# Kernel tuning notes

Hardware: AMD Instinct MI355X
Metric: run time of the kernel (lower is better)

## Reference

```python
import jax, jax.numpy as jnp
import numpy as np

B, N, M_PARAM, F_IN, HEADS, HID, OUT, MLP_H, N_ACT = 64, 512, 50, 3, 2, 3, 3, 128, 512
NEG_SLOPE = 0.2


def setup_inputs() -> dict:
    key = jax.random.key(0)
    ks = jax.random.split(key, 20)
    s = 0.1
    idx = jax.random.uniform(ks[0], (B, N), dtype=jnp.float32)
    x = jax.random.normal(ks[1], (B, N, F_IN), dtype=jnp.float32)
    y = jax.random.normal(ks[2], (B, M_PARAM + 2, F_IN), dtype=jnp.float32)
    adj = (jax.random.uniform(ks[3], (B, N, N)) < 0.02).astype(jnp.float32)
    # GATConv 1: in=3 -> heads=2, out=3 (concat)
    W1 = jax.random.normal(ks[4], (F_IN, HEADS * HID), dtype=jnp.float32) * s
    a_src1 = jax.random.normal(ks[5], (HEADS, HID), dtype=jnp.float32) * s
    a_dst1 = jax.random.normal(ks[6], (HEADS, HID), dtype=jnp.float32) * s
    b1 = jnp.zeros((HEADS * HID,), dtype=jnp.float32)
    # GATConv 2: in=6 -> heads=1, out=3
    W2 = jax.random.normal(ks[7], (HEADS * HID, OUT), dtype=jnp.float32) * s
    a_src2 = jax.random.normal(ks[8], (1, OUT), dtype=jnp.float32) * s
    a_dst2 = jax.random.normal(ks[9], (1, OUT), dtype=jnp.float32) * s
    b2 = jnp.zeros((OUT,), dtype=jnp.float32)
    fc_in = N + N * OUT + (M_PARAM + 2) * 3  # 2204
    Wf1 = jax.random.normal(ks[10], (fc_in, MLP_H), dtype=jnp.float32) * (1.0 / np.sqrt(fc_in))
    bf1 = jnp.zeros((MLP_H,), dtype=jnp.float32)
    Wf2 = jax.random.normal(ks[11], (MLP_H, N_ACT), dtype=jnp.float32) * (1.0 / np.sqrt(MLP_H))
    bf2 = jnp.zeros((N_ACT,), dtype=jnp.float32)
    return {"idx": idx, "x": x, "y": y, "adj": adj,
            "W1": W1, "a_src1": a_src1, "a_dst1": a_dst1, "b1": b1,
            "W2": W2, "a_src2": a_src2, "a_dst2": a_dst2, "b2": b2,
            "Wf1": Wf1, "bf1": bf1, "Wf2": Wf2, "bf2": bf2}


def gat_layer(x, adj, W, a_src, a_dst, bias):
    # PyG GATConv (concat=True): h = x W; alpha_ij = softmax_i(leaky_relu(a_src.h_i + a_dst.h_j))
    # edge (i -> j) exists iff adj[i, j] != 0; self-loops added per PyG default.
    Bb, Nn = x.shape[0], x.shape[1]
    Hh, D = a_src.shape
    h = (x @ W).reshape(Bb, Nn, Hh, D)                     # [B,N,H,D]
    es = jnp.einsum('bnhd,hd->bnh', h, a_src)              # source term
    ed = jnp.einsum('bnhd,hd->bnh', h, a_dst)              # target term
    logits = es[:, :, None, :] + ed[:, None, :, :]         # [B, i(src), j(dst), H]
    logits = jax.nn.leaky_relu(logits, NEG_SLOPE)
    mask = (adj > 0) | jnp.eye(Nn, dtype=bool)[None]       # self-loops
    logits = jnp.where(mask[..., None], logits, jnp.float32(-1e9))
    alpha = jax.nn.softmax(logits, axis=1)                 # softmax over sources per target
    out = jnp.einsum('bijh,bihd->bjhd', alpha, h)          # aggregate at targets
    return out.reshape(Bb, Nn, Hh * D) + bias


def reference(idx, x, y, adj, W1, a_src1, a_dst1, b1, W2, a_src2, a_dst2, b2, Wf1, bf1, Wf2, bf2):
    g = jax.nn.relu(gat_layer(x, adj, W1, a_src1, a_dst1, b1))
    g = gat_layer(g, adj, W2, a_src2, a_dst2, b2)          # heads=1
    feat = jnp.concatenate([idx.reshape(B, -1), g.reshape(B, -1), y.reshape(B, -1)], axis=-1)
    h = jax.nn.relu(feat @ Wf1 + bf1)
    return h @ Wf2 + bf2
```

## Files before the change

kernel.cpp:

```cpp
#include <hip/hip_runtime.h>
#include <hip/hip_bf16.h>
#include <stdint.h>

#define B_    64
#define N_    512
#define M2    52
#define MLPH  128
#define NACT  512
#define FC_IN 2204
#define NCH   18
#define NEG   0.2f
#define NW    16

__device__ __forceinline__ float lrelu(float v){ return v > 0.f ? v : NEG * v; }

__global__ __launch_bounds__(512) void kfuse1(const float* __restrict__ adj,
                                              const float* __restrict__ x,
                                              const float* __restrict__ W1,
                                              const float* __restrict__ as1,
                                              const float* __restrict__ ad1,
                                              const float* __restrict__ b1,
                                              const float* __restrict__ W2,
                                              const float* __restrict__ as2,
                                              uint32_t* __restrict__ maskT,
                                              float* __restrict__ node2){
  __shared__ uint32_t lm[2][64][16];
  __shared__ float node[N_][8];
  int b  = blockIdx.y;
  int j0 = blockIdx.x * 64;
  int t  = threadIdx.x;

  {
    int j4 = t & 15;
    int w  = (t >> 4) & 15;
    int kh = t >> 8;
    const float* basef = adj + ((size_t)(b * N_ + (w << 5) + (kh << 4))) * N_ + (j0 + (j4 << 2));
    uint32_t m0 = 0, m1 = 0, m2 = 0, m3 = 0;
#pragma unroll
    for (int k = 0; k < 16; ++k) {
      float4 v = *(const float4*)(basef + (size_t)k * N_);
      m0 |= (v.x > 0.f ? 1u : 0u) << k;
      m1 |= (v.y > 0.f ? 1u : 0u) << k;
      m2 |= (v.z > 0.f ? 1u : 0u) << k;
      m3 |= (v.w > 0.f ? 1u : 0u) << k;
    }
    int sh = kh << 4;
    lm[kh][(j4 << 2) + 0][w] = m0 << sh;
    lm[kh][(j4 << 2) + 1][w] = m1 << sh;
    lm[kh][(j4 << 2) + 2][w] = m2 << sh;
    lm[kh][(j4 << 2) + 3][w] = m3 << sh;
  }

  {
    float xv0 = x[((size_t)(b * N_ + t)) * 3 + 0];
    float xv1 = x[((size_t)(b * N_ + t)) * 3 + 1];
    float xv2 = x[((size_t)(b * N_ + t)) * 3 + 2];
    float h[6];
#pragma unroll
    for (int c = 0; c < 6; ++c) h[c] = xv0 * W1[c] + xv1 * W1[6 + c] + xv2 * W1[12 + c];
#pragma unroll
    for (int c = 0; c < 6; ++c) node[t][c] = h[c];
    node[t][6] = h[0] * as1[0] + h[1] * as1[1] + h[2] * as1[2];
    node[t][7] = h[3] * as1[3] + h[4] * as1[4] + h[5] * as1[5];
  }
  __syncthreads();

  int w  = t & 15;
  int tg = t >> 4;
  float ad10 = ad1[0], ad11 = ad1[1], ad12 = ad1[2];
  float ad13 = ad1[3], ad14 = ad1[4], ad15 = ad1[5];
  float b10 = b1[0], b11 = b1[1], b12 = b1[2], b13 = b1[3], b14 = b1[4], b15 = b1[5];
  float as20 = as2[0], as21 = as2[1], as22 = as2[2];

#pragma unroll
  for (int p = 0; p < 2; ++p) {
    int jj = tg + p * 32;
    int j  = j0 + jj;
    uint32_t bits = lm[0][jj][w] | lm[1][jj][w];
    maskT[((size_t)(b * N_ + j)) * NW + w] = bits;
    if ((j >> 5) == w) bits |= 1u << (j & 31);

    float ed0 = node[j][0] * ad10 + node[j][1] * ad11 + node[j][2] * ad12;
    float ed1 = node[j][3] * ad13 + node[j][4] * ad14 + node[j][5] * ad15;

    float den0 = 0.f, den1 = 0.f;
    float a0 = 0.f, a1 = 0.f, a2 = 0.f, a3 = 0.f, a4 = 0.f, a5 = 0.f;
    while (bits) {
      int k = __ffs(bits) - 1;
      bits &= bits - 1;
      int i = (w << 5) + k;
      float e0 = __expf(lrelu(node[i][6] + ed0));
      float e1 = __expf(lrelu(node[i][7] + ed1));
      den0 += e0; den1 += e1;
      a0 += e0 * node[i][0]; a1 += e0 * node[i][1]; a2 += e0 * node[i][2];
      a3 += e1 * node[i][3]; a4 += e1 * node[i][4]; a5 += e1 * node[i][5];
    }
#pragma unroll
    for (int m = 1; m < 16; m <<= 1) {
      den0 += __shfl_xor(den0, m); den1 += __shfl_xor(den1, m);
      a0 += __shfl_xor(a0, m); a1 += __shfl_xor(a1, m); a2 += __shfl_xor(a2, m);
      a3 += __shfl_xor(a3, m); a4 += __shfl_xor(a4, m); a5 += __shfl_xor(a5, m);
    }
    float r0 = 1.f / den0, r1 = 1.f / den1;
    float g0 = fmaxf(a0 * r0 + b10, 0.f);
    float g1v = fmaxf(a1 * r0 + b11, 0.f);
    float g2v = fmaxf(a2 * r0 + b12, 0.f);
    float g3 = fmaxf(a3 * r1 + b13, 0.f);
    float g4 = fmaxf(a4 * r1 + b14, 0.f);
    float g5 = fmaxf(a5 * r1 + b15, 0.f);
    float h20 = g0*W2[0] + g1v*W2[3] + g2v*W2[6] + g3*W2[9]  + g4*W2[12] + g5*W2[15];
    float h21 = g0*W2[1] + g1v*W2[4] + g2v*W2[7] + g3*W2[10] + g4*W2[13] + g5*W2[16];
    float h22 = g0*W2[2] + g1v*W2[5] + g2v*W2[8] + g3*W2[11] + g4*W2[14] + g5*W2[17];
    float es2 = h20 * as20 + h21 * as21 + h22 * as22;
    if (w < 4) {
      float outv = (w == 0) ? h20 : (w == 1) ? h21 : (w == 2) ? h22 : es2;
      node2[((size_t)(b * N_ + j)) * 4 + w] = outv;
    }
  }
}

__global__ __launch_bounds__(256) void kagg2(const float* __restrict__ node2,
                                             const float* __restrict__ ad2,
                                             const float* __restrict__ b2,
                                             const uint32_t* __restrict__ maskT,
                                             float* __restrict__ g2){
  __shared__ float sn[N_][4];
  int b = blockIdx.y, tile = blockIdx.x, t = threadIdx.x;

  const float4* src = (const float4*)(node2 + (size_t)b * N_ * 4);
  for (int e = t; e < N_; e += 256) {
    float4 v = src[e];
    sn[e][0] = v.x; sn[e][1] = v.y; sn[e][2] = v.z; sn[e][3] = v.w;
  }
  __syncthreads();

  int w = t & 15, tg = t >> 4;
  int j = tile * 16 + tg;
  float ad20 = ad2[0], ad21 = ad2[1], ad22 = ad2[2];

  uint32_t bits = maskT[((size_t)(b * N_ + j)) * NW + w];
  if ((j >> 5) == w) bits |= 1u << (j & 31);

  float ed = sn[j][0] * ad20 + sn[j][1] * ad21 + sn[j][2] * ad22;
  float den = 0.f, a0 = 0.f, a1 = 0.f, a2 = 0.f;
  while (bits) {
    int k = __ffs(bits) - 1;
    bits &= bits - 1;
    int i = (w << 5) + k;
    float e = __expf(lrelu(sn[i][3] + ed));
    den += e;
    a0 += e * sn[i][0]; a1 += e * sn[i][1]; a2 += e * sn[i][2];
  }
#pragma unroll
  for (int m = 1; m < 16; m <<= 1) {
    den += __shfl_xor(den, m);
    a0 += __shfl_xor(a0, m); a1 += __shfl_xor(a1, m); a2 += __shfl_xor(a2, m);
  }
  if (w < 3) {
    float r = 1.f / den;
    float v = (w == 0 ? a0 : w == 1 ? a1 : a2) * r + b2[w];
    g2[((size_t)(b * N_ + j)) * 3 + w] = v;
  }
}

__global__ __launch_bounds__(128) void kmlp1(const float* __restrict__ idx,
                                             const float* __restrict__ y,
                                             const float* __restrict__ g2,
                                             const float* __restrict__ Wf1,
                                             float* __restrict__ partial){
  __shared__ float fs[128];
  int c = blockIdx.x, b = blockIdx.y, t = threadIdx.x;
  int k = c * 128 + t;
  float v = 0.f;
  if (k < FC_IN) {
    if (k < N_)            v = idx[(size_t)b * N_ + k];
    else if (k < N_ * 4)   v = g2[(size_t)b * (N_ * 3) + (k - N_)];
    else                   v = y[(size_t)b * (M2 * 3) + (k - N_ * 4)];
  }
  fs[t] = v;
  __syncthreads();
  int klen = min(128, FC_IN - c * 128);
  const float* wp = Wf1 + (size_t)(c * 128) * MLPH + t;
  float p = 0.f;
#pragma unroll 8
  for (int kk = 0; kk < klen; ++kk) p += fs[kk] * wp[(size_t)kk * MLPH];
  partial[((size_t)b * NCH + c) * MLPH + t] = p;
}

__global__ __launch_bounds__(128) void kmlp2(const float* __restrict__ partial,
                                             const float* __restrict__ bf1,
                                             const float* __restrict__ Wf2,
                                             const float* __restrict__ bf2,
                                             float* __restrict__ out){
  __shared__ float hid[MLPH];
  int q = blockIdx.x, b = blockIdx.y, t = threadIdx.x;
  float s = bf1[t];
  const float* pp = partial + (size_t)b * NCH * MLPH + t;
#pragma unroll
  for (int c = 0; c < NCH; ++c) s += pp[c * MLPH];
  hid[t] = fmaxf(s, 0.f);
  __syncthreads();
  int o = q * 128 + t;
  float acc = bf2[o];
  const float* wp = Wf2 + o;
#pragma unroll 8
  for (int k = 0; k < MLPH; ++k) acc += hid[k] * wp[(size_t)k * NACT];
  out[(size_t)b * NACT + o] = acc;
}

extern "C" void kernel_launch(void* const* d_in, const int* in_sizes, int n_in,
                              void* d_out, int out_size, void* d_ws, size_t ws_size,
                              hipStream_t stream) {
  const float* idx = (const float*)d_in[0];
  const float* x   = (const float*)d_in[1];
  const float* y   = (const float*)d_in[2];
  const float* adj = (const float*)d_in[3];
  const float* W1  = (const float*)d_in[4];
  const float* as1 = (const float*)d_in[5];
  const float* ad1 = (const float*)d_in[6];
  const float* b1  = (const float*)d_in[7];
  const float* W2  = (const float*)d_in[8];
  const float* as2 = (const float*)d_in[9];
  const float* ad2 = (const float*)d_in[10];
  const float* b2  = (const float*)d_in[11];
  const float* Wf1 = (const float*)d_in[12];
  const float* bf1 = (const float*)d_in[13];
  const float* Wf2 = (const float*)d_in[14];
  const float* bf2 = (const float*)d_in[15];
  float* out = (float*)d_out;

  uint8_t* ws = (uint8_t*)d_ws;
  uint32_t* maskT = (uint32_t*)ws;
  float* node2    = (float*)(ws + 2097152);
  float* g2       = (float*)(ws + 2097152 + 524288);
  float* partial  = (float*)(ws + 2097152 + 524288 + 393216);

  hipLaunchKernelGGL(kfuse1, dim3(8, B_),   dim3(512), 0, stream,
                     adj, x, W1, as1, ad1, b1, W2, as2, maskT, node2);
  hipLaunchKernelGGL(kagg2,  dim3(32, B_),  dim3(256), 0, stream,
                     node2, ad2, b2, maskT, g2);
  hipLaunchKernelGGL(kmlp1,  dim3(NCH, B_), dim3(128), 0, stream, idx, y, g2, Wf1, partial);
  hipLaunchKernelGGL(kmlp2,  dim3(4, B_),   dim3(128), 0, stream, partial, bf1, Wf2, bf2, out);
}
```

Baseline: 38.44 us.

## Fuse second GAT aggregation into first MLP layer kernel

```diff
diff --git a/kernel.cpp b/kernel.cpp
--- a/kernel.cpp
+++ b/kernel.cpp
@@ -119,66 +119,71 @@
   }
 }
 
-__global__ __launch_bounds__(256) void kagg2(const float* __restrict__ node2,
-                                             const float* __restrict__ ad2,
-                                             const float* __restrict__ b2,
-                                             const uint32_t* __restrict__ maskT,
-                                             float* __restrict__ g2){
+__global__ __launch_bounds__(128) void kmlp1f(const float* __restrict__ idx,
+                                              const float* __restrict__ y,
+                                              const float* __restrict__ node2,
+                                              const float* __restrict__ ad2,
+                                              const float* __restrict__ b2,
+                                              const uint32_t* __restrict__ maskT,
+                                              const float* __restrict__ Wf1,
+                                              float* __restrict__ partial){
   __shared__ float sn[N_][4];
-  int b = blockIdx.y, tile = blockIdx.x, t = threadIdx.x;
-
-  const float4* src = (const float4*)(node2 + (size_t)b * N_ * 4);
-  for (int e = t; e < N_; e += 256) {
-    float4 v = src[e];
-    sn[e][0] = v.x; sn[e][1] = v.y; sn[e][2] = v.z; sn[e][3] = v.w;
-  }
-  __syncthreads();
-
-  int w = t & 15, tg = t >> 4;
-  int j = tile * 16 + tg;
-  float ad20 = ad2[0], ad21 = ad2[1], ad22 = ad2[2];
-
-  uint32_t bits = maskT[((size_t)(b * N_ + j)) * NW + w];
-  if ((j >> 5) == w) bits |= 1u << (j & 31);
-
-  float ed = sn[j][0] * ad20 + sn[j][1] * ad21 + sn[j][2] * ad22;
-  float den = 0.f, a0 = 0.f, a1 = 0.f, a2 = 0.f;
-  while (bits) {
-    int k = __ffs(bits) - 1;
-    bits &= bits - 1;
-    int i = (w << 5) + k;
-    float e = __expf(lrelu(sn[i][3] + ed));
-    den += e;
-    a0 += e * sn[i][0]; a1 += e * sn[i][1]; a2 += e * sn[i][2];
-  }
-#pragma unroll
-  for (int m = 1; m < 16; m <<= 1) {
-    den += __shfl_xor(den, m);
-    a0 += __shfl_xor(a0, m); a1 += __shfl_xor(a1, m); a2 += __shfl_xor(a2, m);
-  }
-  if (w < 3) {
-    float r = 1.f / den;
-    float v = (w == 0 ? a0 : w == 1 ? a1 : a2) * r + b2[w];
-    g2[((size_t)(b * N_ + j)) * 3 + w] = v;
-  }
-}
-
-__global__ __launch_bounds__(128) void kmlp1(const float* __restrict__ idx,
-                                             const float* __restrict__ y,
-                                             const float* __restrict__ g2,
-                                             const float* __restrict__ Wf1,
-                                             float* __restrict__ partial){
+  __shared__ float gloc[44][3];
   __shared__ float fs[128];
   int c = blockIdx.x, b = blockIdx.y, t = threadIdx.x;
-  int k = c * 128 + t;
-  float v = 0.f;
-  if (k < FC_IN) {
+
+  if (c >= 4 && c < 16) {
+    const float4* src = (const float4*)(node2 + (size_t)b * N_ * 4);
+    for (int e = t; e < N_; e += 128) {
+      float4 v = src[e];
+      sn[e][0] = v.x; sn[e][1] = v.y; sn[e][2] = v.z; sn[e][3] = v.w;
+    }
+    __syncthreads();
+
+    int kg0 = c * 128 - 512;
+    int j0n = kg0 / 3;
+    int j1n = (kg0 + 127) / 3;
+    int w = t & 15, grp = t >> 4;
+    float ad20 = ad2[0], ad21 = ad2[1], ad22 = ad2[2];
+    float b20 = b2[0], b21 = b2[1], b22 = b2[2];
+
+    for (int jj = j0n + grp; jj <= j1n; jj += 8) {
+      uint32_t bits = maskT[((size_t)(b * N_ + jj)) * NW + w];
+      if ((jj >> 5) == w) bits |= 1u << (jj & 31);
+      float ed = sn[jj][0] * ad20 + sn[jj][1] * ad21 + sn[jj][2] * ad22;
+      float den = 0.f, a0 = 0.f, a1 = 0.f, a2 = 0.f;
+      while (bits) {
+        int k = __ffs(bits) - 1;
+        bits &= bits - 1;
+        int i = (w << 5) + k;
+        float e = __expf(lrelu(sn[i][3] + ed));
+        den += e;
+        a0 += e * sn[i][0]; a1 += e * sn[i][1]; a2 += e * sn[i][2];
+      }
+#pragma unroll
+      for (int m = 1; m < 16; m <<= 1) {
+        den += __shfl_xor(den, m);
+        a0 += __shfl_xor(a0, m); a1 += __shfl_xor(a1, m); a2 += __shfl_xor(a2, m);
+      }
+      if (w < 3) {
+        float r = 1.f / den;
+        float v = (w == 0 ? a0 : w == 1 ? a1 : a2) * r + (w == 0 ? b20 : w == 1 ? b21 : b22);
+        gloc[jj - j0n][w] = v;
+      }
+    }
+    __syncthreads();
+    int kg = kg0 + t;
+    int j = kg / 3, comp = kg - 3 * j;
+    fs[t] = gloc[j - j0n][comp];
+  } else {
+    int k = c * 128 + t;
+    float v = 0.f;
     if (k < N_)            v = idx[(size_t)b * N_ + k];
-    else if (k < N_ * 4)   v = g2[(size_t)b * (N_ * 3) + (k - N_)];
-    else                   v = y[(size_t)b * (M2 * 3) + (k - N_ * 4)];
-  }
-  fs[t] = v;
+    else if (k >= 2048 && k < FC_IN) v = y[(size_t)b * (M2 * 3) + (k - 2048)];
+    fs[t] = v;
+  }
   __syncthreads();
+
   int klen = min(128, FC_IN - c * 128);
   const float* wp = Wf1 + (size_t)(c * 128) * MLPH + t;
   float p = 0.f;
@@ -232,13 +237,12 @@
   uint8_t* ws = (uint8_t*)d_ws;
   uint32_t* maskT = (uint32_t*)ws;
   float* node2    = (float*)(ws + 2097152);
-  float* g2       = (float*)(ws + 2097152 + 524288);
-  float* partial  = (float*)(ws + 2097152 + 524288 + 393216);
+  float* partial  = (float*)(ws + 2097152 + 524288);
 
   hipLaunchKernelGGL(kfuse1, dim3(8, B_),   dim3(512), 0, stream,
                      adj, x, W1, as1, ad1, b1, W2, as2, maskT, node2);
-  hipLaunchKernelGGL(kagg2,  dim3(32, B_),  dim3(256), 0, stream,
-                     node2, ad2, b2, maskT, g2);
-  hipLaunchKernelGGL(kmlp1,  dim3(NCH, B_), dim3(128), 0, stream, idx, y, g2, Wf1, partial);
-  hipLaunchKernelGGL(kmlp2,  dim3(4, B_),   dim3(128), 0, stream, partial, bf1, Wf2, bf2, out);
-}
+  hipLaunchKernelGGL(kmlp1f, dim3(NCH, B_), dim3(128), 0, stream,
+                     idx, y, node2, ad2, b2, maskT, Wf1, partial);
+  hipLaunchKernelGGL(kmlp2,  dim3(4, B_),   dim3(128), 0, stream,
+                     partial, bf1, Wf2, bf2, out);
+}
```

Result: slower. 39.84 us (+3.6%).

## Fuse layer-2 aggregation and both MLP layers into one per-batch kernel

Applied to the files above, without the earlier changes.

```diff
diff --git a/kernel.cpp b/kernel.cpp
--- a/kernel.cpp
+++ b/kernel.cpp
@@ -8,7 +8,6 @@
 #define MLPH  128
 #define NACT  512
 #define FC_IN 2204
-#define NCH   18
 #define NEG   0.2f
 #define NW    16
 
@@ -119,93 +118,116 @@
   }
 }
 
-__global__ __launch_bounds__(256) void kagg2(const float* __restrict__ node2,
-                                             const float* __restrict__ ad2,
-                                             const float* __restrict__ b2,
-                                             const uint32_t* __restrict__ maskT,
-                                             float* __restrict__ g2){
+__global__ __launch_bounds__(1024) void kback(const float* __restrict__ idx,
+                                              const float* __restrict__ y,
+                                              const float* __restrict__ node2,
+                                              const float* __restrict__ ad2,
+                                              const float* __restrict__ b2,
+                                              const uint32_t* __restrict__ maskT,
+                                              const float* __restrict__ Wf1,
+                                              const float* __restrict__ bf1,
+                                              const float* __restrict__ Wf2,
+                                              const float* __restrict__ bf2,
+                                              float* __restrict__ out){
+  __shared__ uint32_t smask[N_][NW];
   __shared__ float sn[N_][4];
-  int b = blockIdx.y, tile = blockIdx.x, t = threadIdx.x;
-
-  const float4* src = (const float4*)(node2 + (size_t)b * N_ * 4);
-  for (int e = t; e < N_; e += 256) {
-    float4 v = src[e];
-    sn[e][0] = v.x; sn[e][1] = v.y; sn[e][2] = v.z; sn[e][3] = v.w;
-  }
-  __syncthreads();
-
-  int w = t & 15, tg = t >> 4;
-  int j = tile * 16 + tg;
-  float ad20 = ad2[0], ad21 = ad2[1], ad22 = ad2[2];
-
-  uint32_t bits = maskT[((size_t)(b * N_ + j)) * NW + w];
-  if ((j >> 5) == w) bits |= 1u << (j & 31);
-
-  float ed = sn[j][0] * ad20 + sn[j][1] * ad21 + sn[j][2] * ad22;
-  float den = 0.f, a0 = 0.f, a1 = 0.f, a2 = 0.f;
-  while (bits) {
-    int k = __ffs(bits) - 1;
-    bits &= bits - 1;
-    int i = (w << 5) + k;
-    float e = __expf(lrelu(sn[i][3] + ed));
-    den += e;
-    a0 += e * sn[i][0]; a1 += e * sn[i][1]; a2 += e * sn[i][2];
-  }
-#pragma unroll
-  for (int m = 1; m < 16; m <<= 1) {
-    den += __shfl_xor(den, m);
-    a0 += __shfl_xor(a0, m); a1 += __shfl_xor(a1, m); a2 += __shfl_xor(a2, m);
-  }
-  if (w < 3) {
-    float r = 1.f / den;
-    float v = (w == 0 ? a0 : w == 1 ? a1 : a2) * r + b2[w];
-    g2[((size_t)(b * N_ + j)) * 3 + w] = v;
-  }
-}
-
-__global__ __launch_bounds__(128) void kmlp1(const float* __restrict__ idx,
-                                             const float* __restrict__ y,
-                                             const float* __restrict__ g2,
-                                             const float* __restrict__ Wf1,
-                                             float* __restrict__ partial){
-  __shared__ float fs[128];
-  int c = blockIdx.x, b = blockIdx.y, t = threadIdx.x;
-  int k = c * 128 + t;
-  float v = 0.f;
-  if (k < FC_IN) {
-    if (k < N_)            v = idx[(size_t)b * N_ + k];
-    else if (k < N_ * 4)   v = g2[(size_t)b * (N_ * 3) + (k - N_)];
-    else                   v = y[(size_t)b * (M2 * 3) + (k - N_ * 4)];
-  }
-  fs[t] = v;
-  __syncthreads();
-  int klen = min(128, FC_IN - c * 128);
-  const float* wp = Wf1 + (size_t)(c * 128) * MLPH + t;
-  float p = 0.f;
+  __shared__ float feat[2208];
+  __shared__ float red[4096];
+  __shared__ float hid[MLPH];
+  int b = blockIdx.x, t = threadIdx.x;
+
+  {
+    const uint4* src = (const uint4*)(maskT + (size_t)b * N_ * NW);
+    uint4* dst = (uint4*)smask;
+    dst[t] = src[t];
+    dst[t + 1024] = src[t + 1024];
+  }
+  if (t < 512) {
+    float4 v = ((const float4*)(node2 + (size_t)b * N_ * 4))[t];
+    sn[t][0] = v.x; sn[t][1] = v.y; sn[t][2] = v.z; sn[t][3] = v.w;
+    feat[t] = idx[(size_t)b * N_ + t];
+  } else if (t < 512 + M2 * 3) {
+    feat[2048 + (t - 512)] = y[(size_t)b * (M2 * 3) + (t - 512)];
+  }
+  __syncthreads();
+
+  {
+    int w = t & 15, jt = t >> 4;
+    float ad20 = ad2[0], ad21 = ad2[1], ad22 = ad2[2];
+    float b20 = b2[0], b21 = b2[1], b22 = b2[2];
+#pragma unroll
+    for (int r = 0; r < 8; ++r) {
+      int j = r * 64 + jt;
+      uint32_t bits = smask[j][w];
+      if ((j >> 5) == w) bits |= 1u << (j & 31);
+      float ed = sn[j][0] * ad20 + sn[j][1] * ad21 + sn[j][2] * ad22;
+      float den = 0.f, a0 = 0.f, a1 = 0.f, a2 = 0.f;
+      while (bits) {
+        int k = __ffs(bits) - 1;
+        bits &= bits - 1;
+        int i = (w << 5) + k;
+        float e = __expf(lrelu(sn[i][3] + ed));
+        den += e;
+        a0 += e * sn[i][0]; a1 += e * sn[i][1]; a2 += e * sn[i][2];
+      }
+#pragma unroll
+      for (int m = 1; m < 16; m <<= 1) {
+        den += __shfl_xor(den, m);
+        a0 += __shfl_xor(a0, m); a1 += __shfl_xor(a1, m); a2 += __shfl_xor(a2, m);
+      }
+      if (w < 3) {
+        float r_ = 1.f / den;
+        float v = (w == 0 ? a0 : w == 1 ? a1 : a2) * r_ + (w == 0 ? b20 : w == 1 ? b21 : b22);
+        feat[N_ + 3 * j + w] = v;
+      }
+    }
+  }
+  __syncthreads();
+
+  {
+    int kq = t >> 5, ug = t & 31;
+    int kstart = kq * 69;
+    int klen = min(69, FC_IN - kstart);
+    const float4* wrow = (const float4*)(Wf1 + (size_t)kstart * MLPH) + ug;
+    float a0 = 0.f, a1 = 0.f, a2 = 0.f, a3 = 0.f;
 #pragma unroll 8
-  for (int kk = 0; kk < klen; ++kk) p += fs[kk] * wp[(size_t)kk * MLPH];
-  partial[((size_t)b * NCH + c) * MLPH + t] = p;
-}
-
-__global__ __launch_bounds__(128) void kmlp2(const float* __restrict__ partial,
-                                             const float* __restrict__ bf1,
-                                             const float* __restrict__ Wf2,
-                                             const float* __restrict__ bf2,
-                                             float* __restrict__ out){
-  __shared__ float hid[MLPH];
-  int q = blockIdx.x, b = blockIdx.y, t = threadIdx.x;
-  float s = bf1[t];
-  const float* pp = partial + (size_t)b * NCH * MLPH + t;
-#pragma unroll
-  for (int c = 0; c < NCH; ++c) s += pp[c * MLPH];
-  hid[t] = fmaxf(s, 0.f);
-  __syncthreads();
-  int o = q * 128 + t;
-  float acc = bf2[o];
-  const float* wp = Wf2 + o;
-#pragma unroll 8
-  for (int k = 0; k < MLPH; ++k) acc += hid[k] * wp[(size_t)k * NACT];
-  out[(size_t)b * NACT + o] = acc;
+    for (int k2 = 0; k2 < 69; ++k2) {
+      if (k2 < klen) {
+        float fv = feat[kstart + k2];
+        float4 w = wrow[(size_t)k2 * 32];
+        a0 += fv * w.x; a1 += fv * w.y; a2 += fv * w.z; a3 += fv * w.w;
+      }
+    }
+    ((float4*)red)[kq * 32 + ug] = make_float4(a0, a1, a2, a3);
+  }
+  __syncthreads();
+  if (t < MLPH) {
+    float s = bf1[t];
+#pragma unroll
+    for (int q = 0; q < 32; ++q) s += red[q * MLPH + t];
+    hid[t] = fmaxf(s, 0.f);
+  }
+  __syncthreads();
+
+  {
+    int kh = t >> 7, og = t & 127;
+    const float4* wrow = (const float4*)(Wf2 + (size_t)(kh * 16) * NACT) + og;
+    float a0 = 0.f, a1 = 0.f, a2 = 0.f, a3 = 0.f;
+#pragma unroll
+    for (int k2 = 0; k2 < 16; ++k2) {
+      float hv = hid[kh * 16 + k2];
+      float4 w = wrow[(size_t)k2 * 128];
+      a0 += hv * w.x; a1 += hv * w.y; a2 += hv * w.z; a3 += hv * w.w;
+    }
+    ((float4*)red)[kh * 128 + og] = make_float4(a0, a1, a2, a3);
+  }
+  __syncthreads();
+  if (t < NACT) {
+    float s = bf2[t];
+#pragma unroll
+    for (int h = 0; h < 8; ++h) s += red[h * NACT + t];
+    out[(size_t)b * NACT + t] = s;
+  }
 }
 
 extern "C" void kernel_launch(void* const* d_in, const int* in_sizes, int n_in,
@@ -232,13 +254,9 @@
   uint8_t* ws = (uint8_t*)d_ws;
   uint32_t* maskT = (uint32_t*)ws;
   float* node2    = (float*)(ws + 2097152);
-  float* g2       = (float*)(ws + 2097152 + 524288);
-  float* partial  = (float*)(ws + 2097152 + 524288 + 393216);
-
-  hipLaunchKernelGGL(kfuse1, dim3(8, B_),   dim3(512), 0, stream,
+
+  hipLaunchKernelGGL(kfuse1, dim3(8, B_), dim3(512), 0, stream,
                      adj, x, W1, as1, ad1, b1, W2, as2, maskT, node2);
-  hipLaunchKernelGGL(kagg2,  dim3(32, B_),  dim3(256), 0, stream,
-                     node2, ad2, b2, maskT, g2);
-  hipLaunchKernelGGL(kmlp1,  dim3(NCH, B_), dim3(128), 0, stream, idx, y, g2, Wf1, partial);
-  hipLaunchKernelGGL(kmlp2,  dim3(4, B_),   dim3(128), 0, stream, partial, bf1, Wf2, bf2, out);
+  hipLaunchKernelGGL(kback,  dim3(B_),    dim3(1024), 0, stream,
+                     idx, y, node2, ad2, b2, maskT, Wf1, bf1, Wf2, bf2, out);
 }
```

Result: slower. 54.35 us (+41.4%).
